# Kernel optimization log

Measured on AMD Instinct MI355X. Metric: run time of the kernel, lower is better.

## Reference

```python
import jax, jax.numpy as jnp
import numpy as np

EPS = 1e-9
THRESHOLD = 0.5


def _spatial_entropy(feat, w1, b1, w2, b2):
    # feat: [B, C, H, W]
    p = jax.nn.sigmoid(feat)
    # faithful to source: log(p+eps) - (1-p)*log(1-p+eps)
    ent = jnp.log(p + EPS) - (1.0 - p) * jnp.log(1.0 - p + EPS)  # [B,C,H,W]
    pooled = feat.mean(axis=(2, 3))                               # [B,C]
    h = jax.nn.relu(pooled @ w1 + b1)                             # [B,64]
    cw = jax.nn.sigmoid(h @ w2 + b2)                              # [B,C]
    se = jnp.einsum('bchw,bc->bhw', ent, cw)                      # [B,H,W]
    # F.normalize(x, dim=(1,2)): L2-normalize jointly over H,W
    norm = jnp.sqrt(jnp.sum(se * se, axis=(1, 2), keepdims=True))
    return se / jnp.maximum(norm, 1e-12)


def _low_entropy_mask(entropy_map):
    # entropy_map: [B,H,W] -> mask [B,1,H,W]
    thr = entropy_map.mean(axis=(1, 2), keepdims=True) * THRESHOLD
    return (entropy_map < thr).astype(entropy_map.dtype)[:, None, :, :]


def setup_inputs() -> dict:
    key = jax.random.key(0)
    k1, k2, k3, k4 = jax.random.split(key, 4)
    B, C, H, W = 16, 256, 64, 64
    vis_feat = jax.random.normal(k1, (B, C, H, W), dtype=jnp.float32)
    text_feat = jax.random.normal(k2, (B, C, H, W), dtype=jnp.float32)
    # channel attention MLP params (Linear(256,64) -> Linear(64,256))
    w1 = jax.random.normal(k3, (256, 64), dtype=jnp.float32) * 0.0625
    b1 = jnp.zeros((64,), dtype=jnp.float32)
    w2 = jax.random.normal(k4, (64, 256), dtype=jnp.float32) * 0.125
    b2 = jnp.zeros((256,), dtype=jnp.float32)
    return {"vis_feat": vis_feat, "text_feat": text_feat,
            "w1": w1, "b1": b1, "w2": w2, "b2": b2}


def reference(vis_feat, text_feat, w1, b1, w2, b2):
    vis_entropy = _spatial_entropy(vis_feat, w1, b1, w2, b2)    # [B,H,W]
    text_entropy = _spatial_entropy(text_feat, w1, b1, w2, b2)  # [B,H,W]
    vis_low = _low_entropy_mask(vis_entropy)                     # [B,1,H,W]
    text_low = _low_entropy_mask(text_entropy)                   # [B,1,H,W]
    enhanced = vis_feat * vis_low + text_feat * text_low * (1.0 - vis_low)
    return enhanced, vis_entropy, text_entropy
```

## Files before the change

### kernel.cpp

```cpp
#include <hip/hip_runtime.h>
#include <math.h>

#define B 16
#define C 256
#define HW 4096
#define EPSE 1e-9f
#define NTHREADS 256
#define CCHUNK 16

typedef float nfloat4 __attribute__((ext_vector_type(4)));

__device__ __forceinline__ void nt_store4(float* p, float4 v) {
    nfloat4 nv = { v.x, v.y, v.z, v.w };
    __builtin_nontemporal_store(nv, (nfloat4*)p);
}

__device__ __forceinline__ float fast_rcp(float x) { return __builtin_amdgcn_rcpf(x); }

__device__ __forceinline__ float entf(float x) {
    float e  = __expf(-x);
    float p  = fast_rcp(1.f + e);
    float l1 = __logf(p + EPSE);
    float q  = 1.f - p;
    float l2 = __logf(q + EPSE);
    return fmaf(-q, l2, l1);
}

__global__ void k_pooled(const float* __restrict__ vis,
                         const float* __restrict__ txt,
                         float* __restrict__ pooled,
                         float* __restrict__ se) {
    int row = blockIdx.x;
    if (row < 128)
        ((float4*)se)[row * NTHREADS + threadIdx.x] = make_float4(0.f, 0.f, 0.f, 0.f);

    int f  = row >> 12;
    int bc = row & (B * C - 1);
    const float* src = (f == 0 ? vis : txt) + (size_t)bc * HW + threadIdx.x * 4;

    float4 a = *(const float4*)(src + 0);
    float4 b = *(const float4*)(src + 1024);
    float4 c = *(const float4*)(src + 2048);
    float4 d = *(const float4*)(src + 3072);
    float s = (((a.x + a.y) + (a.z + a.w)) + ((b.x + b.y) + (b.z + b.w)))
            + (((c.x + c.y) + (c.z + c.w)) + ((d.x + d.y) + (d.z + d.w)));

    for (int off = 32; off > 0; off >>= 1) s += __shfl_down(s, off);
    __shared__ float sm[4];
    if ((threadIdx.x & 63) == 0) sm[threadIdx.x >> 6] = s;
    __syncthreads();
    if (threadIdx.x == 0)
        pooled[row] = (sm[0] + sm[1] + sm[2] + sm[3]) * (1.0f / HW);
}

__global__ void __launch_bounds__(NTHREADS, 4)
k_se(const float* __restrict__ vis,
     const float* __restrict__ txt,
     const float* __restrict__ pooled,
     const float* __restrict__ w1, const float* __restrict__ b1,
     const float* __restrict__ w2, const float* __restrict__ b2,
     float* __restrict__ se) {
    __shared__ float pl[C];
    __shared__ float h[64];
    __shared__ float cwl[CCHUNK];

    const int tid  = threadIdx.x;
    int bx   = blockIdx.x;
    int cc   = bx & 15;
    int tile = (bx >> 4) & 3;
    int b    = (bx >> 6) & 15;
    int f    = bx >> 10;

    pl[tid] = pooled[(f * B + b) * C + tid];
    __syncthreads();

    if (tid < 64) {
        float acc = b1[tid];
        const float* w1p = w1 + tid;
        #pragma unroll 8
        for (int c2 = 0; c2 < C; ++c2)
            acc = fmaf(pl[c2], w1p[(size_t)c2 * 64], acc);
        h[tid] = fmaxf(acc, 0.f);
    }
    __syncthreads();
    if (tid < CCHUNK) {
        int c2 = cc * CCHUNK + tid;
        float acc = b2[c2];
        #pragma unroll 8
        for (int j = 0; j < 64; ++j)
            acc = fmaf(h[j], w2[j * 256 + c2], acc);
        cwl[tid] = fast_rcp(1.f + __expf(-acc));
    }
    __syncthreads();

    const float* src = (f == 0 ? vis : txt)
                       + (size_t)b * C * HW + (size_t)cc * CCHUNK * HW
                       + tile * 1024 + tid * 4;

    float4 acc = make_float4(0.f, 0.f, 0.f, 0.f);
    #pragma unroll
    for (int g = 0; g < CCHUNK / 8; ++g) {
        float4 xs[8];
        #pragma unroll
        for (int j = 0; j < 8; ++j)
            xs[j] = *(const float4*)(src + (size_t)(g * 8 + j) * HW);
        #pragma unroll
        for (int j = 0; j < 8; ++j) {
            float w = cwl[g * 8 + j];
            acc.x = fmaf(entf(xs[j].x), w, acc.x);
            acc.y = fmaf(entf(xs[j].y), w, acc.y);
            acc.z = fmaf(entf(xs[j].z), w, acc.z);
            acc.w = fmaf(entf(xs[j].w), w, acc.w);
        }
    }
    float* dst = se + (size_t)(f * B + b) * HW + tile * 1024 + tid * 4;
    atomicAdd(dst + 0, acc.x);
    atomicAdd(dst + 1, acc.y);
    atomicAdd(dst + 2, acc.z);
    atomicAdd(dst + 3, acc.w);
}

__global__ void __launch_bounds__(NTHREADS, 4)
k_final(const float* __restrict__ vis,
        const float* __restrict__ txt,
        const float* __restrict__ se,
        float* __restrict__ out_enh,
        float* __restrict__ out_ent_vis,
        float* __restrict__ out_ent_text) {
    const int tid = threadIdx.x;
    int bx   = blockIdx.x;
    int cg   = bx & 15;
    int tile = (bx >> 4) & 3;
    int b    = bx >> 6;

    const float4* s0 = (const float4*)(se + (size_t)b * HW);
    const float4* s1 = (const float4*)(se + (size_t)(B + b) * HW);
    float su0 = 0.f, sq0 = 0.f, su1 = 0.f, sq1 = 0.f;
    #pragma unroll
    for (int i = tid; i < HW / 4; i += NTHREADS) {
        float4 v = s0[i];
        su0 += v.x + v.y + v.z + v.w;
        sq0 = fmaf(v.x, v.x, sq0); sq0 = fmaf(v.y, v.y, sq0);
        sq0 = fmaf(v.z, v.z, sq0); sq0 = fmaf(v.w, v.w, sq0);
        float4 w = s1[i];
        su1 += w.x + w.y + w.z + w.w;
        sq1 = fmaf(w.x, w.x, sq1); sq1 = fmaf(w.y, w.y, sq1);
        sq1 = fmaf(w.z, w.z, sq1); sq1 = fmaf(w.w, w.w, sq1);
    }
    #pragma unroll
    for (int off = 32; off > 0; off >>= 1) {
        su0 += __shfl_down(su0, off);
        sq0 += __shfl_down(sq0, off);
        su1 += __shfl_down(su1, off);
        sq1 += __shfl_down(sq1, off);
    }
    __shared__ float sred[16];
    __shared__ float bcv[4];
    if ((tid & 63) == 0) {
        int w = tid >> 6;
        sred[w * 4 + 0] = su0; sred[w * 4 + 1] = sq0;
        sred[w * 4 + 2] = su1; sred[w * 4 + 3] = sq1;
    }
    __syncthreads();
    if (tid == 0) {
        float st0  = sred[0] + sred[4] + sred[8]  + sred[12];
        float sst0 = sred[1] + sred[5] + sred[9]  + sred[13];
        float st1  = sred[2] + sred[6] + sred[10] + sred[14];
        float sst1 = sred[3] + sred[7] + sred[11] + sred[15];
        bcv[0] = 0.5f * (st0 * (1.0f / HW));
        bcv[1] = 0.5f * (st1 * (1.0f / HW));
        bcv[2] = 1.f / fmaxf(sqrtf(sst0), 1e-12f);
        bcv[3] = 1.f / fmaxf(sqrtf(sst1), 1e-12f);
    }
    __syncthreads();
    float tv = bcv[0], tt = bcv[1];

    int hw   = tile * 1024 + tid * 4;
    int mapi = b * HW + hw;

    float4 sv = *(const float4*)(se + mapi);
    float4 st = *(const float4*)(se + B * HW + mapi);

    if (cg == 0) {
        float inv = bcv[2], int_ = bcv[3];
        float4 ov = make_float4(sv.x * inv, sv.y * inv, sv.z * inv, sv.w * inv);
        float4 ot = make_float4(st.x * int_, st.y * int_, st.z * int_, st.w * int_);
        nt_store4(out_ent_vis + mapi, ov);
        nt_store4(out_ent_text + mapi, ot);
    }

    int m0 = sv.x < tv ? 1 : (st.x < tt ? 2 : 0);
    int m1 = sv.y < tv ? 1 : (st.y < tt ? 2 : 0);
    int m2 = sv.z < tv ? 1 : (st.z < tt ? 2 : 0);
    int m3 = sv.w < tv ? 1 : (st.w < tt ? 2 : 0);

    size_t base = (size_t)b * C * HW + (size_t)cg * 16 * HW + hw;
    #pragma unroll
    for (int g = 0; g < 2; ++g) {
        float4 vv[8], tt4[8];
        #pragma unroll
        for (int c = 0; c < 8; ++c) {
            size_t idx = base + (size_t)(g * 8 + c) * HW;
            vv[c]  = *(const float4*)(vis + idx);
            tt4[c] = *(const float4*)(txt + idx);
        }
        #pragma unroll
        for (int c = 0; c < 8; ++c) {
            size_t idx = base + (size_t)(g * 8 + c) * HW;
            float4 o;
            o.x = (m0 == 1) ? vv[c].x : ((m0 == 2) ? tt4[c].x : 0.f);
            o.y = (m1 == 1) ? vv[c].y : ((m1 == 2) ? tt4[c].y : 0.f);
            o.z = (m2 == 1) ? vv[c].z : ((m2 == 2) ? tt4[c].z : 0.f);
            o.w = (m3 == 1) ? vv[c].w : ((m3 == 2) ? tt4[c].w : 0.f);
            nt_store4(out_enh + idx, o);
        }
    }
}

extern "C" void kernel_launch(void* const* d_in, const int* in_sizes, int n_in,
                              void* d_out, int out_size, void* d_ws, size_t ws_size,
                              hipStream_t stream) {
    const float* vis = (const float*)d_in[0];
    const float* txt = (const float*)d_in[1];
    const float* w1  = (const float*)d_in[2];
    const float* b1  = (const float*)d_in[3];
    const float* w2  = (const float*)d_in[4];
    const float* b2  = (const float*)d_in[5];

    float* out_enh      = (float*)d_out;
    float* out_ent_vis  = out_enh + (size_t)B * C * HW;
    float* out_ent_text = out_ent_vis + B * HW;

    float* ws     = (float*)d_ws;
    float* pooled = ws;
    float* se     = ws + 8192;

    k_pooled<<<8192, NTHREADS, 0, stream>>>(vis, txt, pooled, se);
    k_se    <<<2048, NTHREADS, 0, stream>>>(vis, txt, pooled,
                                            w1, b1, w2, b2, se);
    k_final <<<1024, NTHREADS, 0, stream>>>(vis, txt, se,
                                            out_enh, out_ent_vis, out_ent_text);
}
```

Baseline: 245.1 us.

## Simplify entropy math and hoist channel MLP into a separate kernel

Rewrites the per-element entropy using softplus identities so it needs one exp, one log and one reciprocal instead of two logs, dropping the epsilon terms. Moves the channel-attention MLP out of every k_se block into a dedicated two-block kernel that writes channel weights to workspace. This removes redundant MLP recomputation and transcendental work in the hot loop. The cost is an extra launch and a serial low-parallelism MLP stage, and the eps-free formula can overflow for very negative inputs.

```diff
diff --git a/kernel.cpp b/kernel.cpp
--- a/kernel.cpp
+++ b/kernel.cpp
@@ -4,7 +4,6 @@
 #define B 16
 #define C 256
 #define HW 4096
-#define EPSE 1e-9f
 #define NTHREADS 256
 #define CCHUNK 16
 
@@ -18,12 +17,11 @@
 __device__ __forceinline__ float fast_rcp(float x) { return __builtin_amdgcn_rcpf(x); }
 
 __device__ __forceinline__ float entf(float x) {
-    float e  = __expf(-x);
-    float p  = fast_rcp(1.f + e);
-    float l1 = __logf(p + EPSE);
-    float q  = 1.f - p;
-    float l2 = __logf(q + EPSE);
-    return fmaf(-q, l2, l1);
+    float t = __expf(-x);
+    float u = 1.f + t;
+    float L = __logf(u);
+    float r = fast_rcp(u);
+    return fmaf(t * r, x + L, -L);
 }
 
 __global__ void k_pooled(const float* __restrict__ vis,
@@ -53,49 +51,49 @@
         pooled[row] = (sm[0] + sm[1] + sm[2] + sm[3]) * (1.0f / HW);
 }
 
+__global__ void k_mlp(const float* __restrict__ pooled,
+                      const float* __restrict__ w1, const float* __restrict__ b1,
+                      const float* __restrict__ w2, const float* __restrict__ b2,
+                      float* __restrict__ cw) {
+    __shared__ float pl[B * C];
+    __shared__ float h[B * 64];
+    int f = blockIdx.x;
+    const float* P = pooled + f * B * C;
+    for (int i = threadIdx.x; i < B * C; i += NTHREADS) pl[i] = P[i];
+    __syncthreads();
+    for (int o = threadIdx.x; o < B * 64; o += NTHREADS) {
+        int b = o >> 6, j = o & 63;
+        float acc = b1[j];
+        for (int c = 0; c < C; ++c) acc = fmaf(pl[b * C + c], w1[c * 64 + j], acc);
+        h[o] = fmaxf(acc, 0.f);
+    }
+    __syncthreads();
+    for (int o = threadIdx.x; o < B * C; o += NTHREADS) {
+        int b = o >> 8, c2 = o & 255;
+        float acc = b2[c2];
+        for (int j = 0; j < 64; ++j) acc = fmaf(h[b * 64 + j], w2[j * 256 + c2], acc);
+        cw[f * B * C + o] = fast_rcp(1.f + __expf(-acc));
+    }
+}
+
 __global__ void __launch_bounds__(NTHREADS, 4)
 k_se(const float* __restrict__ vis,
      const float* __restrict__ txt,
-     const float* __restrict__ pooled,
-     const float* __restrict__ w1, const float* __restrict__ b1,
-     const float* __restrict__ w2, const float* __restrict__ b2,
+     const float* __restrict__ cw,
      float* __restrict__ se) {
-    __shared__ float pl[C];
-    __shared__ float h[64];
-    __shared__ float cwl[CCHUNK];
-
-    const int tid  = threadIdx.x;
     int bx   = blockIdx.x;
     int cc   = bx & 15;
     int tile = (bx >> 4) & 3;
     int b    = (bx >> 6) & 15;
     int f    = bx >> 10;
-
-    pl[tid] = pooled[(f * B + b) * C + tid];
-    __syncthreads();
-
-    if (tid < 64) {
-        float acc = b1[tid];
-        const float* w1p = w1 + tid;
-        #pragma unroll 8
-        for (int c2 = 0; c2 < C; ++c2)
-            acc = fmaf(pl[c2], w1p[(size_t)c2 * 64], acc);
-        h[tid] = fmaxf(acc, 0.f);
-    }
-    __syncthreads();
-    if (tid < CCHUNK) {
-        int c2 = cc * CCHUNK + tid;
-        float acc = b2[c2];
-        #pragma unroll 8
-        for (int j = 0; j < 64; ++j)
-            acc = fmaf(h[j], w2[j * 256 + c2], acc);
-        cwl[tid] = fast_rcp(1.f + __expf(-acc));
-    }
-    __syncthreads();
-
     const float* src = (f == 0 ? vis : txt)
                        + (size_t)b * C * HW + (size_t)cc * CCHUNK * HW
-                       + tile * 1024 + tid * 4;
+                       + tile * 1024 + threadIdx.x * 4;
+
+    __shared__ float cwl[CCHUNK];
+    if (threadIdx.x < CCHUNK)
+        cwl[threadIdx.x] = cw[f * B * C + b * C + cc * CCHUNK + threadIdx.x];
+    __syncthreads();
 
     float4 acc = make_float4(0.f, 0.f, 0.f, 0.f);
     #pragma unroll
@@ -113,7 +111,7 @@
             acc.w = fmaf(entf(xs[j].w), w, acc.w);
         }
     }
-    float* dst = se + (size_t)(f * B + b) * HW + tile * 1024 + tid * 4;
+    float* dst = se + (size_t)(f * B + b) * HW + tile * 1024 + threadIdx.x * 4;
     atomicAdd(dst + 0, acc.x);
     atomicAdd(dst + 1, acc.y);
     atomicAdd(dst + 2, acc.z);
@@ -233,11 +231,12 @@
 
     float* ws     = (float*)d_ws;
     float* pooled = ws;
-    float* se     = ws + 8192;
+    float* cw     = ws + 8192;
+    float* se     = ws + 16384;
 
     k_pooled<<<8192, NTHREADS, 0, stream>>>(vis, txt, pooled, se);
-    k_se    <<<2048, NTHREADS, 0, stream>>>(vis, txt, pooled,
-                                            w1, b1, w2, b2, se);
+    k_mlp   <<<2,    NTHREADS, 0, stream>>>(pooled, w1, b1, w2, b2, cw);
+    k_se    <<<2048, NTHREADS, 0, stream>>>(vis, txt, cw, se);
     k_final <<<1024, NTHREADS, 0, stream>>>(vis, txt, se,
                                             out_enh, out_ent_vis, out_ent_text);
 }
```

Result: slower. 258.8 us (+5.6%).
